# Optimization experiments

Measured on AMD Instinct MI355X. Metric: run time of the kernel, lower is better.

Reference implementation:

```python
import jax, jax.numpy as jnp
import numpy as np

N = 20000      # nodes
E = 80000      # edges (before self loops)
NG = 64        # graphs in batch
EMB = 780      # embedding_size (768 text + 12 time)
NEG_SLOPE = 0.2
BN_EPS = 1e-5


def setup_inputs() -> dict:
    key = jax.random.key(0)
    ks = jax.random.split(key, 20)
    def rn(k, shape, s=0.05):
        return jax.random.normal(k, shape, dtype=jnp.float32) * s
    z = lambda n: jnp.zeros((n,), dtype=jnp.float32)
    o = lambda n: jnp.ones((n,), dtype=jnp.float32)
    x = jax.random.normal(ks[0], (N, 772), dtype=jnp.float32)
    edge_index = jax.random.randint(ks[1], (2, E), 0, N)
    batch = jnp.sort(jax.random.randint(ks[2], (N,), 0, NG))
    return dict(
        x=x, edge_index=edge_index, batch=batch,
        time_W=rn(ks[3], (4, 12)), time_b=z(12),
        lin_W0=rn(ks[4], (EMB, 3 * EMB)), att_src0=rn(ks[5], (3, EMB)), att_dst0=rn(ks[6], (3, EMB)),
        bias0=z(3 * EMB), gamma0=o(3 * EMB), beta0=z(3 * EMB),
        lin_W1=rn(ks[7], (3 * EMB, 3 * EMB)), att_src1=rn(ks[8], (3, EMB)), att_dst1=rn(ks[9], (3, EMB)),
        bias1=z(3 * EMB), gamma1=o(3 * EMB), beta1=z(3 * EMB),
        lin_W2=rn(ks[10], (3 * EMB, EMB)), att_src2=rn(ks[11], (1, EMB)), att_dst2=rn(ks[12], (1, EMB)),
        bias2=z(EMB), gamma2=o(EMB), beta2=z(EMB),
        mlp_W1=rn(ks[13], (EMB, 128)), mlp_b1=z(128),
        mlp_W2=rn(ks[14], (128, 64)), mlp_b2=z(64),
    )


def _gat_layer(h, src, dst, W, a_src, a_dst, b, heads):
    # PyG GATConv (eval mode: dropout off), concat=True, self loops already in src/dst
    C = W.shape[1] // heads
    hp = (h @ W).reshape(N, heads, C)                       # [N,H,C]
    a_s = jnp.sum(hp * a_src[None], axis=-1)                # [N,H]
    a_d = jnp.sum(hp * a_dst[None], axis=-1)                # [N,H]
    e = jax.nn.leaky_relu(a_s[src] + a_d[dst], NEG_SLOPE)   # [E+N,H]
    m = jax.ops.segment_max(e, dst, num_segments=N)         # segment softmax over incoming edges
    m = jnp.where(jnp.isfinite(m), m, 0.0)
    p = jnp.exp(e - m[dst])
    denom = jax.ops.segment_sum(p, dst, num_segments=N)
    alpha = p / (denom[dst] + 1e-16)                        # [E+N,H]
    out = jax.ops.segment_sum(alpha[:, :, None] * hp[src], dst, num_segments=N)  # [N,H,C]
    return out.reshape(N, heads * C) + b


def _bn(h, gamma, beta):
    # BatchNorm in training-mode math (batch statistics, biased variance)
    mu = jnp.mean(h, axis=0)
    var = jnp.mean((h - mu) ** 2, axis=0)
    return (h - mu) * jax.lax.rsqrt(var + BN_EPS) * gamma + beta


def reference(x, edge_index, batch, time_W, time_b,
              lin_W0, att_src0, att_dst0, bias0, gamma0, beta0,
              lin_W1, att_src1, att_dst1, bias1, gamma1, beta1,
              lin_W2, att_src2, att_dst2, bias2, gamma2, beta2,
              mlp_W1, mlp_b1, mlp_W2, mlp_b2):
    te = x[:, 768:772] @ time_W + time_b
    h = jnp.concatenate([jax.lax.stop_gradient(x[:, :768]), te,
                         jax.lax.stop_gradient(x[:, 772:])], axis=-1)  # [N, 780]
    sl = jnp.arange(N)
    src = jnp.concatenate([edge_index[0], sl])   # add self loops
    dst = jnp.concatenate([edge_index[1], sl])
    layers = [
        (lin_W0, att_src0, att_dst0, bias0, gamma0, beta0, 3),
        (lin_W1, att_src1, att_dst1, bias1, gamma1, beta1, 3),
        (lin_W2, att_src2, att_dst2, bias2, gamma2, beta2, 1),
    ]
    for W, a_s, a_d, b, g, bt, heads in layers:
        h = jnp.tanh(_gat_layer(h, src, dst, W, a_s, a_d, b, heads))
        h = _bn(h, g, bt)
    cnt = jax.ops.segment_sum(jnp.ones((N,), dtype=h.dtype), batch, num_segments=NG)
    pooled = jax.ops.segment_sum(h, batch, num_segments=NG) / jnp.maximum(cnt, 1.0)[:, None]
    pooled = jax.nn.relu(pooled)
    out = jnp.tanh(pooled @ mlp_W1 + mlp_b1) @ mlp_W2 + mlp_b2
    return out  # [NG, 64]
```

## Files before the change

### kernel.cpp

```cpp
#include <hip/hip_runtime.h>
#include <math.h>

#define NN   20000
#define EE   80000
#define ELP  100000
#define NGR  64
#define EMB  780
#define W3   2340
#define EMBP 832
#define W3P  2368
#define NZ   (W3+8)

static inline int cdiv_i(long long a, long long b){ return (int)((a + b - 1) / b); }

typedef _Float16 f16;
typedef _Float16 f16x4 __attribute__((ext_vector_type(4)));
typedef _Float16 f16x8 __attribute__((ext_vector_type(8)));
typedef float    f32x4 __attribute__((ext_vector_type(4)));

__device__ __forceinline__ void async_ld16(const f16* g, f16* l){
    __builtin_amdgcn_global_load_lds(
        (const __attribute__((address_space(1))) unsigned int*)g,
        (__attribute__((address_space(3))) unsigned int*)l,
        16, 0, 0);
}

__global__ void k_zero_f32(float* p, int n){
    int i = blockIdx.x*256 + threadIdx.x; if (i < n) p[i] = 0.f;
}
__global__ void k_zero_i32(int* p, int n){
    int i = blockIdx.x*256 + threadIdx.x; if (i < n) p[i] = 0;
}

__global__ void k_transpose(const float* __restrict__ W, f16* __restrict__ Wt,
                            const float* __restrict__ sc, const float* __restrict__ sh,
                            float* __restrict__ dvec, int K, int N, int KP){
    __shared__ float T[32][33];
    __shared__ float D[8][33];
    int n0 = blockIdx.x*32, k0 = blockIdx.y*32;
    int tx = threadIdx.x, ty = threadIdx.y;
    float raw[4];
#pragma unroll
    for (int r = 0; r < 4; r++){
        int k = k0 + ty + r*8;
        float w = 0.f;
        if (k < K && n0 + tx < N) w = W[(size_t)k*N + n0 + tx];
        raw[r] = w;
        T[ty + r*8][tx] = sc ? w * ((k < K) ? sc[k] : 0.f) : w;
    }
    if (sh){
        float p = 0.f;
#pragma unroll
        for (int r = 0; r < 4; r++){
            int k = k0 + ty + r*8;
            if (k < K) p += sh[k] * raw[r];
        }
        D[ty][tx] = p;
    }
    __syncthreads();
#pragma unroll
    for (int r = 0; r < 4; r++){
        int n = n0 + ty + r*8;
        int k = k0 + tx;
        if (n < N && k < KP) Wt[(size_t)n*KP + k] = (f16)T[tx][ty + r*8];
    }
    if (sh && ty == 0 && n0 + tx < N){
        float s = 0.f;
#pragma unroll
        for (int j = 0; j < 8; j++) s += D[j][tx];
        atomicAdd(&dvec[n0 + tx], s);
    }
}

__global__ void k_wvec(const float* __restrict__ W, const float* __restrict__ asrc,
                       const float* __restrict__ adst, const float* __restrict__ sc,
                       f16* __restrict__ Wt, float* __restrict__ dvec,
                       int K, int N, int KP, int H){
    int k = blockIdx.x*4 + (threadIdx.x >> 6);
    int lane = threadIdx.x & 63;
    if (k < K){
        const float* row = W + (size_t)k*N;
        float acc[6];
#pragma unroll
        for (int i = 0; i < 6; i++) acc[i] = 0.f;
        for (int c = lane; c < EMB; c += 64){
            for (int h = 0; h < H; h++){
                float wv = row[h*EMB + c];
                acc[h]     += wv * asrc[h*EMB + c];
                acc[H + h] += wv * adst[h*EMB + c];
            }
        }
        float s = sc ? sc[k] : 1.f;
        for (int i = 0; i < 2*H; i++){
            float v = acc[i];
#pragma unroll
            for (int off = 32; off; off >>= 1) v += __shfl_xor(v, off);
            if (lane == 0) Wt[(size_t)(N + i)*KP + k] = (f16)(v * s);
        }
    }
    if (blockIdx.x == 0){
        int wv = threadIdx.x >> 6;
        for (int i = wv; i < 2*H; i += 4){
            int h = (i < H) ? i : (i - H);
            const float* att = (i < H) ? (asrc + h*EMB) : (adst + h*EMB);
            float s = 0.f;
            for (int c = lane; c < EMB; c += 64) s += dvec[h*EMB + c] * att[c];
#pragma unroll
            for (int off = 32; off; off >>= 1) s += __shfl_xor(s, off);
            if (lane == 0) dvec[N + i] = s;
        }
    }
}

__global__ void k_build_h(const float* __restrict__ x, const float* __restrict__ tW,
                          const float* __restrict__ tb, f16* __restrict__ h){
    int idx = blockIdx.x*256 + threadIdx.x;
    int total = NN*(EMBP/4);
    if (idx >= total) return;
    int n = idx / (EMBP/4);
    int c0 = (idx - n*(EMBP/4))*4;
    const float* xr = x + (size_t)n*772;
    f16x4 o;
#pragma unroll
    for (int j = 0; j < 4; j++){
        int c = c0 + j; float v;
        if (c < 768) v = xr[c];
        else if (c < EMB){
            int t = c - 768;
            v = tb[t] + xr[768]*tW[t] + xr[769]*tW[12+t] + xr[770]*tW[24+t] + xr[771]*tW[36+t];
        } else v = 0.f;
        o[j] = (f16)v;
    }
    *(f16x4*)(h + (size_t)n*EMBP + c0) = o;
}

__global__ void k_deg(const int* __restrict__ ei, int* __restrict__ deg){
    int k = blockIdx.x*256 + threadIdx.x; if (k >= ELP) return;
    int d = (k < EE) ? ei[EE + k] : (k - EE);
    atomicAdd(&deg[d], 1);
}

__global__ __launch_bounds__(1024) void k_scan(int* __restrict__ deg, int* __restrict__ rp){
    __shared__ int part[1024];
    int tid = threadIdx.x;
    int i0 = tid*20;
    int n = (i0 < NN) ? min(20, NN - i0) : 0;
    int s = 0;
    for (int k = 0; k < n; k++) s += deg[i0+k];
    part[tid] = s; __syncthreads();
    for (int off = 1; off < 1024; off <<= 1){
        int t = (tid >= off) ? part[tid-off] : 0;
        __syncthreads();
        part[tid] += t;
        __syncthreads();
    }
    int run = part[tid] - s;
    for (int k = 0; k < n; k++){
        int d = deg[i0+k];
        rp[i0+k] = run;
        deg[i0+k] = run;
        run += d;
    }
    if (tid == 1023) rp[NN] = part[1023];
}

__global__ void k_fill(const int* __restrict__ ei, int* __restrict__ cursor, int* __restrict__ csrc){
    int k = blockIdx.x*256 + threadIdx.x; if (k >= ELP) return;
    int s, d;
    if (k < EE){ s = ei[k]; d = ei[EE + k]; } else { s = k - EE; d = s; }
    int pos = atomicAdd(&cursor[d], 1);
    csrc[pos] = s;
}

__global__ void k_grp(const int* __restrict__ batch, int* __restrict__ grp){
    int g = blockIdx.x*256 + threadIdx.x; if (g > NGR) return;
    int lo = 0, hi = NN;
    while (lo < hi){ int mid = (lo+hi)>>1; if (batch[mid] < g) lo = mid+1; else hi = mid; }
    grp[g] = lo;
}

__global__ __launch_bounds__(512, 4) void k_gemmT(const f16* __restrict__ A,
                                                  const f16* __restrict__ Bt,
                                                  const float* __restrict__ dvec,
                                                  f16* __restrict__ C,
                                                  float* __restrict__ a_sd,
                                                  int M, int N, int NB, int H,
                                                  int KP, int SN, int Mtiles, int NT){
    __shared__ f16 smem[36864];
    f16* sB = smem + 12288;

    int nwg = Mtiles*NT;
    int bid = blockIdx.x;
    int q = nwg >> 3, r = nwg & 7, xcd = bid & 7, lin = bid >> 3;
    int wg = (xcd < r ? xcd*(q+1) : r*(q+1) + (xcd - r)*q) + lin;
    int mt = wg / NT, nt = wg - mt*NT;
    int m0 = mt*128, n0 = nt*256;

    int tid = threadIdx.x;
    int w = tid >> 6, lane = tid & 63;
    int lm = lane & 15, lq = lane >> 4;
    int wm = w >> 2, wn = w & 3;

    int kqs = ((lane & 3) ^ ((lane >> 3) & 3)) * 8;
    const f16* gA0 = A  + (size_t)min(m0 + w*16 + (lane >> 2), M-1)*KP + kqs;
    const f16* gB0 = Bt + (size_t)min(n0 + w*32 + (lane >> 2), NB-1)*KP + kqs;
    const f16* gB1 = Bt + (size_t)min(n0 + w*32 + 16 + (lane >> 2), NB-1)*KP + kqs;
    int sa0 = w*512;
    int sb0 = w*1024, sb1 = w*1024 + 512;

    int swz  = (lq ^ ((lm >> 1) & 3)) * 8;
    int aoff = (wm*64 + lm)*32 + swz;
    int boff = (wn*64 + lm)*32 + swz;

    f32x4 acc[4][4];
#pragma unroll
    for (int i = 0; i < 4; i++)
#pragma unroll
        for (int j = 0; j < 4; j++) acc[i][j] = (f32x4)0.f;

    int KT = KP >> 5;

    async_ld16(gA0,      &smem[sa0]);
    async_ld16(gB0,      &sB[sb0]);
    async_ld16(gB1,      &sB[sb1]);
    async_ld16(gA0 + 32, &smem[4096 + sa0]);
    async_ld16(gB0 + 32, &sB[8192 + sb0]);
    async_ld16(gB1 + 32, &sB[8192 + sb1]);
    asm volatile("s_waitcnt vmcnt(3)" ::: "memory");
    __builtin_amdgcn_s_barrier();

    int cur = 0, nx2 = 2;
    for (int t = 0; t < KT; t++){
        int ac = cur*4096, bc = cur*8192;
        f16x8 aF[4], bF[4];
#pragma unroll
        for (int i = 0; i < 4; i++) aF[i] = *(const f16x8*)&smem[ac + aoff + i*512];
#pragma unroll
        for (int i = 0; i < 4; i++) bF[i] = *(const f16x8*)&sB[bc + boff + i*512];
        bool s2 = (t+2 < KT);
        if (s2){
            int ko2 = (t+2)*32;
            int a2 = nx2*4096, b2 = nx2*8192;
            async_ld16(gA0 + ko2, &smem[a2 + sa0]);
            async_ld16(gB0 + ko2, &sB[b2 + sb0]);
            async_ld16(gB1 + ko2, &sB[b2 + sb1]);
        }
        __builtin_amdgcn_s_setprio(1);
#pragma unroll
        for (int i = 0; i < 4; i++)
#pragma unroll
            for (int j = 0; j < 4; j++)
                acc[i][j] = __builtin_amdgcn_mfma_f32_16x16x32_f16(aF[i], bF[j], acc[i][j], 0, 0, 0);
        __builtin_amdgcn_s_setprio(0);
        if (s2) asm volatile("s_waitcnt vmcnt(3)" ::: "memory");
        else    asm volatile("s_waitcnt vmcnt(0)" ::: "memory");
        __builtin_amdgcn_s_barrier();
        cur = (cur == 2) ? 0 : cur + 1;
        nx2 = (nx2 == 2) ? 0 : nx2 + 1;
    }

#pragma unroll
    for (int mi = 0; mi < 4; mi++){
#pragma unroll
        for (int ni = 0; ni < 4; ni++){
            int col = n0 + wn*64 + ni*16 + lm;
            if (col >= N && col < NB){
                int jc = col - N;
                int idx = (jc < H) ? jc : (3 + jc - H);
                float dv = dvec[col];
                int rbase = m0 + wm*64 + mi*16 + lq*4;
#pragma unroll
                for (int rr = 0; rr < 4; rr++){
                    int row = rbase + rr;
                    if (row < M) a_sd[(size_t)row*6 + idx] = acc[mi][ni][rr] + dv;
                }
            }
        }
    }

    float dv4[4];
#pragma unroll
    for (int ni = 0; ni < 4; ni++){
        int gcol = n0 + wn*64 + ni*16 + lm;
        dv4[ni] = (gcol < N) ? dvec[gcol] : 0.f;
    }
    int ncols = min(256, N - n0);
#pragma unroll
    for (int mi = 0; mi < 4; mi++){
#pragma unroll
        for (int ni = 0; ni < 4; ni++){
            int colL = wn*64 + ni*16 + lm;
#pragma unroll
            for (int rr = 0; rr < 4; rr++){
                int rowL = wm*64 + mi*16 + lq*4 + rr;
                smem[rowL*264 + colL] = (f16)(acc[mi][ni][rr] + dv4[ni]);
            }
        }
    }
    asm volatile("s_waitcnt lgkmcnt(0)" ::: "memory");
    __builtin_amdgcn_s_barrier();
#pragma unroll
    for (int it = 0; it < 8; it++){
        int ch = tid + it*512;
        int rowL = ch >> 5, cc = (ch & 31)*8;
        int grow = m0 + rowL;
        if (grow < M && cc < ncols){
            if (cc + 8 <= ncols){
                f16x8 v = *(f16x8*)&smem[rowL*264 + cc];
                *(f16x8*)(C + (size_t)grow*SN + n0 + cc) = v;
            } else {
                for (int jj = cc; jj < ncols; jj++)
                    C[(size_t)grow*SN + n0 + jj] = smem[rowL*264 + jj];
            }
        }
    }
}

template<int H, int NG>
__global__ __launch_bounds__(256) void k_agg3(const f16* __restrict__ hp, const int* __restrict__ rp,
                                              const int* __restrict__ csrc, const float* __restrict__ a_sd,
                                              const float* __restrict__ bias,
                                              f16* __restrict__ y, int SP, int W){
    int n = blockIdx.x*4 + (threadIdx.x >> 6);
    if (n >= NN) return;
    int lane = threadIdx.x & 63;
    int beg = rp[n], deg = rp[n+1] - beg;

    float adv[H];
#pragma unroll
    for (int h = 0; h < H; h++) adv[h] = a_sd[(size_t)n*6 + 3 + h];

    bool act0 = lane < deg;
    int sl0 = 0;
    float t0[H];
    if (act0){
        sl0 = csrc[beg + lane];
#pragma unroll
        for (int h = 0; h < H; h++){
            float t = a_sd[(size_t)sl0*6 + h] + adv[h];
            t0[h] = t > 0.f ? t : 0.2f*t;
        }
    } else {
#pragma unroll
        for (int h = 0; h < H; h++) t0[h] = -1e30f;
    }

    float mx[H];
#pragma unroll
    for (int h = 0; h < H; h++) mx[h] = t0[h];
    for (int base = 64; base < deg; base += 64){
        int e = base + lane;
        if (e < deg){
            int s = csrc[beg + e];
#pragma unroll
            for (int h = 0; h < H; h++){
                float t = a_sd[(size_t)s*6 + h] + adv[h];
                t = t > 0.f ? t : 0.2f*t;
                mx[h] = fmaxf(mx[h], t);
            }
        }
    }
#pragma unroll
    for (int off = 32; off; off >>= 1)
#pragma unroll
        for (int h = 0; h < H; h++) mx[h] = fmaxf(mx[h], __shfl_xor(mx[h], off));

    float dn[H];
#pragma unroll
    for (int h = 0; h < H; h++) dn[h] = act0 ? expf(t0[h] - mx[h]) : 0.f;
    for (int base = 64; base < deg; base += 64){
        int e = base + lane;
        if (e < deg){
            int s = csrc[beg + e];
#pragma unroll
            for (int h = 0; h < H; h++){
                float t = a_sd[(size_t)s*6 + h] + adv[h];
                t = t > 0.f ? t : 0.2f*t;
                dn[h] += expf(t - mx[h]);
            }
        }
    }
#pragma unroll
    for (int off = 32; off; off >>= 1)
#pragma unroll
        for (int h = 0; h < H; h++) dn[h] += __shfl_xor(dn[h], off);
    float inv[H];
#pragma unroll
    for (int h = 0; h < H; h++) inv[h] = 1.f / (dn[h] + 1e-16f);

    float acc[NG][8];
    int  hlo[NG], hhi[NG], nsp[NG];
    bool cok[NG];
    int  cbase[NG];
#pragma unroll
    for (int g = 0; g < NG; g++){
        int c = g*512 + lane*8;
        cbase[g] = c;
        cok[g] = c < SP;
        int hl = min(c / EMB, H-1);
        int hh = min((c+7) / EMB, H-1);
        hlo[g] = hl; hhi[g] = hh;
        nsp[g] = (hh > hl) ? (EMB*(hl+1) - c) : 8;
#pragma unroll
        for (int j = 0; j < 8; j++) acc[g][j] = 0.f;
    }

    for (int base = 0; base < deg; base += 64){
        int cnt = min(64, deg - base);
        int sl; float al[H];
        if (base == 0){
            sl = sl0;
#pragma unroll
            for (int h = 0; h < H; h++) al[h] = act0 ? expf(t0[h] - mx[h]) * inv[h] : 0.f;
        } else {
            int e = base + lane;
            sl = 0;
#pragma unroll
            for (int h = 0; h < H; h++) al[h] = 0.f;
            if (e < deg){
                sl = csrc[beg + e];
#pragma unroll
                for (int h = 0; h < H; h++){
                    float t = a_sd[(size_t)sl*6 + h] + adv[h];
                    t = t > 0.f ? t : 0.2f*t;
                    al[h] = expf(t - mx[h]) * inv[h];
                }
            }
        }
#pragma unroll 4
        for (int e = 0; e < cnt; e++){
            int s = __shfl(sl, e);
            float a0 = __shfl(al[0], e);
            float a1 = (H==3) ? __shfl(al[1], e) : a0;
            float a2 = (H==3) ? __shfl(al[2], e) : a0;
            const f16* row = hp + (size_t)s*SP;
#pragma unroll
            for (int g = 0; g < NG; g++){
                if (cok[g]){
                    f16x8 v = *(const f16x8*)(row + cbase[g]);
                    float lo = (H==3) ? ((hlo[g]==0) ? a0 : ((hlo[g]==1) ? a1 : a2)) : a0;
                    float hi = (H==3) ? ((hhi[g]==0) ? a0 : ((hhi[g]==1) ? a1 : a2)) : a0;
#pragma unroll
                    for (int j = 0; j < 8; j++){
                        float alj = (j < nsp[g]) ? lo : hi;
                        acc[g][j] += alj * (float)v[j];
                    }
                }
            }
        }
    }

#pragma unroll
    for (int g = 0; g < NG; g++){
        if (cok[g]){
            int c = cbase[g];
            f16x8 o;
#pragma unroll
            for (int j = 0; j < 8; j++){
                float vv = (c + j < W) ? tanhf(acc[g][j] + bias[c+j]) : 0.f;
                o[j] = (f16)vv;
            }
            *(f16x8*)(y + (size_t)n*SP + c) = o;
        }
    }
}

__global__ void k_bnstat(const f16* __restrict__ y, float* __restrict__ ps,
                         float* __restrict__ pq, int W, int SP){
    int c0 = (blockIdx.x*256 + threadIdx.x)*4;
    if (c0 >= W) return;
    int slice = blockIdx.y;
    int r0 = (int)(((long long)NN*slice)/128);
    int r1 = (int)(((long long)NN*(slice+1))/128);
    float s[4] = {0,0,0,0}, q[4] = {0,0,0,0};
    for (int r = r0; r < r1; r++){
        f16x4 u = *(const f16x4*)(y + (size_t)r*SP + c0);
#pragma unroll
        for (int j = 0; j < 4; j++){ float v = (float)u[j]; s[j] += v; q[j] += v*v; }
    }
#pragma unroll
    for (int j = 0; j < 4; j++){
        ps[(size_t)slice*W3 + c0+j] = s[j];
        pq[(size_t)slice*W3 + c0+j] = q[j];
    }
}

__global__ void k_bnfin(const float* __restrict__ ps, const float* __restrict__ pq,
                        const float* __restrict__ gamma, const float* __restrict__ beta,
                        float* __restrict__ sc, float* __restrict__ sh,
                        float* __restrict__ dvec, int W, int zn){
    int c = blockIdx.x*256 + threadIdx.x;
    if (c < W){
        float m = 0.f, q = 0.f;
        for (int s = 0; s < 128; s++){ m += ps[(size_t)s*W3 + c]; q += pq[(size_t)s*W3 + c]; }
        m *= (1.f/NN);
        float v = q * (1.f/NN) - m*m;
        float is = 1.f / sqrtf(v + 1e-5f);
        float g = gamma[c];
        sc[c] = is * g;
        sh[c] = beta[c] - m * is * g;
    }
    if (c < zn) dvec[c] = 0.f;
}

__global__ void k_pool(const f16* __restrict__ h, const int* __restrict__ grp,
                       float* __restrict__ pooled){
    int g = blockIdx.x;
    int c = threadIdx.x*4;
    if (c >= EMB) return;
    int r0 = grp[g], r1 = grp[g+1];
    float s0=0.f, s1=0.f, s2=0.f, s3=0.f;
    for (int r = r0; r < r1; r++){
        f16x4 u = *(const f16x4*)(h + (size_t)r*EMBP + c);
        s0 += (float)u[0]; s1 += (float)u[1]; s2 += (float)u[2]; s3 += (float)u[3];
    }
    pooled[g*EMB + c] = s0; pooled[g*EMB + c+1] = s1;
    pooled[g*EMB + c+2] = s2; pooled[g*EMB + c+3] = s3;
}

__global__ __launch_bounds__(256) void k_mlp(const float* __restrict__ pooled, const int* __restrict__ grp,
                                             const float* __restrict__ sc, const float* __restrict__ sh,
                                             const float* __restrict__ W1, const float* __restrict__ b1,
                                             const float* __restrict__ W2, const float* __restrict__ b2,
                                             float* __restrict__ out){
    __shared__ float p[EMB];
    __shared__ float hid[128];
    int g = blockIdx.x, tid = threadIdx.x;
    int cnt = grp[g+1] - grp[g];
    float ic = 1.f / fmaxf((float)cnt, 1.f);
    for (int c = tid; c < EMB; c += 256){
        float v = pooled[g*EMB + c] * ic * sc[c] + sh[c];
        p[c] = v > 0.f ? v : 0.f;
    }
    __syncthreads();
    if (tid < 128){
        float s = b1[tid];
        for (int k = 0; k < EMB; k++) s += p[k] * W1[k*128 + tid];
        hid[tid] = tanhf(s);
    }
    __syncthreads();
    if (tid < 64){
        float s = b2[tid];
        for (int k = 0; k < 128; k++) s += hid[k] * W2[k*64 + tid];
        out[g*64 + tid] = s;
    }
}

extern "C" void kernel_launch(void* const* d_in, const int* in_sizes, int n_in,
                              void* d_out, int out_size, void* d_ws, size_t ws_size,
                              hipStream_t stream) {
    (void)in_sizes; (void)n_in; (void)out_size;
    const float* x    = (const float*)d_in[0];
    const int*   ei   = (const int*)  d_in[1];
    const int*   batch= (const int*)  d_in[2];
    const float* tW   = (const float*)d_in[3];
    const float* tb   = (const float*)d_in[4];
    const float* W0   = (const float*)d_in[5];
    const float* as0  = (const float*)d_in[6];
    const float* ad0  = (const float*)d_in[7];
    const float* b0   = (const float*)d_in[8];
    const float* g0   = (const float*)d_in[9];
    const float* be0  = (const float*)d_in[10];
    const float* W1   = (const float*)d_in[11];
    const float* as1  = (const float*)d_in[12];
    const float* ad1  = (const float*)d_in[13];
    const float* b1   = (const float*)d_in[14];
    const float* g1   = (const float*)d_in[15];
    const float* be1  = (const float*)d_in[16];
    const float* W2   = (const float*)d_in[17];
    const float* as2  = (const float*)d_in[18];
    const float* ad2  = (const float*)d_in[19];
    const float* b2   = (const float*)d_in[20];
    const float* g2   = (const float*)d_in[21];
    const float* be2  = (const float*)d_in[22];
    const float* mW1  = (const float*)d_in[23];
    const float* mb1  = (const float*)d_in[24];
    const float* mW2  = (const float*)d_in[25];
    const float* mb2  = (const float*)d_in[26];
    float* outp = (float*)d_out;

    size_t off = 0;
    auto carve = [&](size_t bytes) -> void* {
        void* p = (char*)d_ws + off;
        off = (off + bytes + 255) & ~(size_t)255;
        return p;
    };
    f16* big1 = (f16*)carve((size_t)NN*W3P*2);
    f16* big2 = (f16*)carve((size_t)NN*W3P*2);
    f16* Wt   = (f16*)carve((size_t)NZ*W3P*2);
    float* a_sd  = (float*)carve((size_t)NN*6*4);
    float* psum  = (float*)carve((size_t)128*W3*4);
    float* psq   = (float*)carve((size_t)128*W3*4);
    float* sc    = (float*)carve((size_t)W3*4);
    float* sh    = (float*)carve((size_t)W3*4);
    float* dvec  = (float*)carve((size_t)NZ*4);
    float* pooled= (float*)carve((size_t)NGR*EMB*4);
    int*   grp   = (int*)carve((size_t)(NGR+1)*4);
    int*   deg   = (int*)carve((size_t)NN*4);
    int*   rp    = (int*)carve((size_t)(NN+1)*4);
    int*   csrc  = (int*)carve((size_t)ELP*4);

    if (ws_size < off) return;

    k_zero_i32<<<cdiv_i(NN,256),256,0,stream>>>(deg, NN);
    k_deg<<<cdiv_i(ELP,256),256,0,stream>>>(ei, deg);
    k_scan<<<1,1024,0,stream>>>(deg, rp);
    k_fill<<<cdiv_i(ELP,256),256,0,stream>>>(ei, deg, csrc);
    k_grp<<<1,256,0,stream>>>(batch, grp);

    k_build_h<<<cdiv_i((long long)NN*(EMBP/4),256),256,0,stream>>>(x, tW, tb, big1);
    k_zero_f32<<<cdiv_i(NZ,256),256,0,stream>>>(dvec, NZ);

    struct Layer { const float* W; const float* as; const float* ad; const float* b;
                   const float* g; const float* be; int H; int K; int KP; };
    Layer layers[3] = {
        {W0, as0, ad0, b0, g0, be0, 3, EMB, EMBP},
        {W1, as1, ad1, b1, g1, be1, 3, W3,  W3P },
        {W2, as2, ad2, b2, g2, be2, 1, W3,  W3P },
    };

    for (int L = 0; L < 3; L++){
        Layer& ly = layers[L];
        int Wout  = ly.H * EMB;
        int NB    = Wout + 2*ly.H;
        int SPout = (Wout == W3) ? W3P : EMBP;
        const float* scale = (L == 0) ? nullptr : sc;
        const float* shift = (L == 0) ? nullptr : sh;

        dim3 tg(cdiv_i(Wout,32), cdiv_i(ly.KP,32));
        k_transpose<<<tg, dim3(32,8), 0, stream>>>(ly.W, Wt, scale, shift, dvec, ly.K, Wout, ly.KP);
        k_wvec<<<cdiv_i(ly.K,4),256,0,stream>>>(ly.W, ly.as, ly.ad, scale, Wt, dvec, ly.K, Wout, ly.KP, ly.H);

        int Mtiles = cdiv_i(NN,128), NT = cdiv_i(NB,256);
        k_gemmT<<<Mtiles*NT, 512, 0, stream>>>(big1, Wt, dvec, big2, a_sd,
                                               NN, Wout, NB, ly.H, ly.KP, SPout, Mtiles, NT);

        if (ly.H == 3)
            k_agg3<3,5><<<cdiv_i(NN,4),256,0,stream>>>(big2, rp, csrc, a_sd, ly.b, big1, SPout, Wout);
        else
            k_agg3<1,2><<<cdiv_i(NN,4),256,0,stream>>>(big2, rp, csrc, a_sd, ly.b, big1, SPout, Wout);

        dim3 gs(cdiv_i(Wout/4,256), 128);
        k_bnstat<<<gs,256,0,stream>>>(big1, psum, psq, Wout, SPout);
        int zn = (L < 2) ? NZ : 0;
        k_bnfin<<<cdiv_i(Wout,256),256,0,stream>>>(psum, psq, ly.g, ly.be, sc, sh, dvec, Wout, zn);
    }

    k_pool<<<NGR,256,0,stream>>>(big1, grp, pooled);
    k_mlp<<<NGR,256,0,stream>>>(pooled, grp, sc, sh, mW1, mb1, mW2, mb2, outp);
}
```

Measured before the change: 1.436 ms.

## Split GAT aggregation into alpha kernel and column-parallel gather kernel

Splits the fused softmax-plus-aggregation kernel in two. The first kernel computes normalized attention coefficients per edge and stores them in a new buffer. The second gathers neighbor rows with one 512-column slice per grid y-block, so each thread keeps only 8 accumulators and the grid exposes more parallelism. The cost is an extra launch, an alpha round-trip through memory, and csrc reads repeated for every column slice.

```diff
diff --git a/kernel.cpp b/kernel.cpp
--- a/kernel.cpp
+++ b/kernel.cpp
@@ -316,11 +316,9 @@
     }
 }
 
-template<int H, int NG>
-__global__ __launch_bounds__(256) void k_agg3(const f16* __restrict__ hp, const int* __restrict__ rp,
-                                              const int* __restrict__ csrc, const float* __restrict__ a_sd,
-                                              const float* __restrict__ bias,
-                                              f16* __restrict__ y, int SP, int W){
+template<int H>
+__global__ __launch_bounds__(256) void k_alpha(const int* __restrict__ rp, const int* __restrict__ csrc,
+                                               const float* __restrict__ a_sd, float* __restrict__ alpha){
     int n = blockIdx.x*4 + (threadIdx.x >> 6);
     if (n >= NN) return;
     int lane = threadIdx.x & 63;
@@ -331,8 +329,7 @@
     for (int h = 0; h < H; h++) adv[h] = a_sd[(size_t)n*6 + 3 + h];
 
     bool act0 = lane < deg;
-    int sl0 = 0;
-    float t0[H];
+    int sl0 = 0; float t0[H];
     if (act0){
         sl0 = csrc[beg + lane];
 #pragma unroll
@@ -388,80 +385,98 @@
 #pragma unroll
     for (int h = 0; h < H; h++) inv[h] = 1.f / (dn[h] + 1e-16f);
 
-    float acc[NG][8];
-    int  hlo[NG], hhi[NG], nsp[NG];
-    bool cok[NG];
-    int  cbase[NG];
-#pragma unroll
-    for (int g = 0; g < NG; g++){
-        int c = g*512 + lane*8;
-        cbase[g] = c;
-        cok[g] = c < SP;
-        int hl = min(c / EMB, H-1);
-        int hh = min((c+7) / EMB, H-1);
-        hlo[g] = hl; hhi[g] = hh;
-        nsp[g] = (hh > hl) ? (EMB*(hl+1) - c) : 8;
-#pragma unroll
-        for (int j = 0; j < 8; j++) acc[g][j] = 0.f;
-    }
+    if (act0){
+        if (H == 3){
+            float4 o;
+            o.x = expf(t0[0]-mx[0])*inv[0];
+            o.y = expf(t0[1]-mx[1])*inv[1];
+            o.z = expf(t0[2]-mx[2])*inv[2];
+            o.w = 0.f;
+            *(float4*)(alpha + (size_t)(beg+lane)*4) = o;
+        } else {
+            alpha[beg+lane] = expf(t0[0]-mx[0])*inv[0];
+        }
+    }
+    for (int base = 64; base < deg; base += 64){
+        int e = base + lane;
+        if (e < deg){
+            int s = csrc[beg + e];
+            float av[H];
+#pragma unroll
+            for (int h = 0; h < H; h++){
+                float t = a_sd[(size_t)s*6 + h] + adv[h];
+                t = t > 0.f ? t : 0.2f*t;
+                av[h] = expf(t - mx[h]) * inv[h];
+            }
+            if (H == 3){
+                float4 o; o.x = av[0]; o.y = av[1]; o.z = av[2]; o.w = 0.f;
+                *(float4*)(alpha + (size_t)(beg+e)*4) = o;
+            } else {
+                alpha[beg+e] = av[0];
+            }
+        }
+    }
+}
+
+template<int H>
+__global__ __launch_bounds__(256) void k_gather(const f16* __restrict__ hp, const int* __restrict__ rp,
+                                                const int* __restrict__ csrc, const float* __restrict__ alpha,
+                                                const float* __restrict__ bias, f16* __restrict__ y,
+                                                int SP, int W){
+    int w = threadIdx.x >> 6, lane = threadIdx.x & 63;
+    int n = blockIdx.x*4 + w;
+    if (n >= NN) return;
+    int c = blockIdx.y*512 + lane*8;
+    bool cok = c < SP;
+    int beg = rp[n], deg = rp[n+1] - beg;
+
+    int hl = 0, hh = 0, nsp = 8;
+    if (H == 3){
+        hl = min(c/EMB, 2); hh = min((c+7)/EMB, 2);
+        nsp = (hh > hl) ? (EMB*(hl+1) - c) : 8;
+    }
+    float acc[8];
+#pragma unroll
+    for (int j = 0; j < 8; j++) acc[j] = 0.f;
 
     for (int base = 0; base < deg; base += 64){
         int cnt = min(64, deg - base);
-        int sl; float al[H];
-        if (base == 0){
-            sl = sl0;
-#pragma unroll
-            for (int h = 0; h < H; h++) al[h] = act0 ? expf(t0[h] - mx[h]) * inv[h] : 0.f;
-        } else {
-            int e = base + lane;
-            sl = 0;
-#pragma unroll
-            for (int h = 0; h < H; h++) al[h] = 0.f;
-            if (e < deg){
-                sl = csrc[beg + e];
-#pragma unroll
-                for (int h = 0; h < H; h++){
-                    float t = a_sd[(size_t)sl*6 + h] + adv[h];
-                    t = t > 0.f ? t : 0.2f*t;
-                    al[h] = expf(t - mx[h]) * inv[h];
-                }
+        int e0 = base + lane;
+        int sl = 0; float a0v = 0.f, a1v = 0.f, a2v = 0.f;
+        if (e0 < deg){
+            sl = csrc[beg + e0];
+            if (H == 3){
+                float4 al4 = *(const float4*)(alpha + (size_t)(beg+e0)*4);
+                a0v = al4.x; a1v = al4.y; a2v = al4.z;
+            } else {
+                a0v = alpha[beg + e0];
             }
         }
 #pragma unroll 4
         for (int e = 0; e < cnt; e++){
             int s = __shfl(sl, e);
-            float a0 = __shfl(al[0], e);
-            float a1 = (H==3) ? __shfl(al[1], e) : a0;
-            float a2 = (H==3) ? __shfl(al[2], e) : a0;
-            const f16* row = hp + (size_t)s*SP;
-#pragma unroll
-            for (int g = 0; g < NG; g++){
-                if (cok[g]){
-                    f16x8 v = *(const f16x8*)(row + cbase[g]);
-                    float lo = (H==3) ? ((hlo[g]==0) ? a0 : ((hlo[g]==1) ? a1 : a2)) : a0;
-                    float hi = (H==3) ? ((hhi[g]==0) ? a0 : ((hhi[g]==1) ? a1 : a2)) : a0;
-#pragma unroll
-                    for (int j = 0; j < 8; j++){
-                        float alj = (j < nsp[g]) ? lo : hi;
-                        acc[g][j] += alj * (float)v[j];
-                    }
-                }
-            }
-        }
-    }
-
-#pragma unroll
-    for (int g = 0; g < NG; g++){
-        if (cok[g]){
-            int c = cbase[g];
-            f16x8 o;
-#pragma unroll
-            for (int j = 0; j < 8; j++){
-                float vv = (c + j < W) ? tanhf(acc[g][j] + bias[c+j]) : 0.f;
-                o[j] = (f16)vv;
-            }
-            *(f16x8*)(y + (size_t)n*SP + c) = o;
-        }
+            float b0 = __shfl(a0v, e);
+            float b1 = (H==3) ? __shfl(a1v, e) : b0;
+            float b2 = (H==3) ? __shfl(a2v, e) : b0;
+            if (cok){
+                f16x8 v = *(const f16x8*)(hp + (size_t)s*SP + c);
+                float lo = (H==3) ? ((hl==0)?b0:((hl==1)?b1:b2)) : b0;
+                float hi = (H==3) ? ((hh==0)?b0:((hh==1)?b1:b2)) : b0;
+#pragma unroll
+                for (int j = 0; j < 8; j++)
+                    acc[j] += ((j < nsp) ? lo : hi) * (float)v[j];
+            }
+        }
+    }
+
+    if (cok){
+        f16x8 o;
+#pragma unroll
+        for (int j = 0; j < 8; j++){
+            float vv = (c + j < W) ? tanhf(acc[j] + bias[c+j]) : 0.f;
+            o[j] = (f16)vv;
+        }
+        *(f16x8*)(y + (size_t)n*SP + c) = o;
     }
 }
 
@@ -594,6 +609,7 @@
     float* sc    = (float*)carve((size_t)W3*4);
     float* sh    = (float*)carve((size_t)W3*4);
     float* dvec  = (float*)carve((size_t)NZ*4);
+    float* alphab= (float*)carve((size_t)ELP*4*4);
     float* pooled= (float*)carve((size_t)NGR*EMB*4);
     int*   grp   = (int*)carve((size_t)(NGR+1)*4);
     int*   deg   = (int*)carve((size_t)NN*4);
@@ -635,10 +651,14 @@
         k_gemmT<<<Mtiles*NT, 512, 0, stream>>>(big1, Wt, dvec, big2, a_sd,
                                                NN, Wout, NB, ly.H, ly.KP, SPout, Mtiles, NT);
 
-        if (ly.H == 3)
-            k_agg3<3,5><<<cdiv_i(NN,4),256,0,stream>>>(big2, rp, csrc, a_sd, ly.b, big1, SPout, Wout);
-        else
-            k_agg3<1,2><<<cdiv_i(NN,4),256,0,stream>>>(big2, rp, csrc, a_sd, ly.b, big1, SPout, Wout);
+        dim3 gg(cdiv_i(NN,4), cdiv_i(SPout,512));
+        if (ly.H == 3){
+            k_alpha<3><<<cdiv_i(NN,4),256,0,stream>>>(rp, csrc, a_sd, alphab);
+            k_gather<3><<<gg,256,0,stream>>>(big2, rp, csrc, alphab, ly.b, big1, SPout, Wout);
+        } else {
+            k_alpha<1><<<cdiv_i(NN,4),256,0,stream>>>(rp, csrc, a_sd, alphab);
+            k_gather<1><<<gg,256,0,stream>>>(big2, rp, csrc, alphab, ly.b, big1, SPout, Wout);
+        }
 
         dim3 gs(cdiv_i(Wout/4,256), 128);
         k_bnstat<<<gs,256,0,stream>>>(big1, psum, psq, Wout, SPout);
```

Result: faster. 1.400 ms (-2.6%).
